# Kernel optimization log

Measured on AMD Instinct MI355X. Metric: run time of the kernel, lower is better.

Reference implementation:

```python
import jax, jax.numpy as jnp
import numpy as np

B, N, E, D = 32, 512, 2048, 128
N_STEPS = 3


def setup_inputs() -> dict:
    key = jax.random.key(0)
    ks = jax.random.split(key, 16)
    s = 0.05
    return {
        "prop_state": jax.random.normal(ks[0], (B, N, D), jnp.float32),
        "edge_states": jax.random.normal(ks[1], (B, E, D), jnp.float32),
        "A": jax.random.uniform(ks[2], (B, N, E), jnp.float32) / E,
        "tem_features": jax.random.normal(ks[3], (B, 64), jnp.float32),
        "link_W": jax.random.normal(ks[4], (D, D), jnp.float32) * s,
        "link_b": jnp.zeros((D,), jnp.float32),
        "reset_W": jax.random.normal(ks[5], (2 * D, D), jnp.float32) * s,
        "reset_b": jnp.zeros((D,), jnp.float32),
        "update_W": jax.random.normal(ks[6], (2 * D, D), jnp.float32) * s,
        "update_b": jnp.zeros((D,), jnp.float32),
        "trans_W": jax.random.normal(ks[7], (2 * D, D), jnp.float32) * s,
        "trans_b": jnp.zeros((D,), jnp.float32),
        "att_W1": jax.random.normal(ks[8], (D, D), jnp.float32) * s,
        "att_b1": jnp.zeros((D,), jnp.float32),
        "att_W2": jax.random.normal(ks[9], (D, 1), jnp.float32) * s,
        "att_b2": jnp.zeros((1,), jnp.float32),
        "out_W": jax.random.normal(ks[10], (D, D), jnp.float32) * s,
        "out_b": jnp.zeros((D,), jnp.float32),
    }


def reference(prop_state, edge_states, A, tem_features,
              link_W, link_b, reset_W, reset_b, update_W, update_b,
              trans_W, trans_b, att_W1, att_b1, att_W2, att_b2, out_W, out_b):
    init_node = prop_state
    init_edge = edge_states
    for _ in range(N_STEPS):
        edge_states = edge_states @ link_W + link_b              # [B,E,D]
        a_cur = jnp.einsum('bne,bed->bnd', A, edge_states)       # [B,N,D]
        a = jnp.concatenate([a_cur, prop_state], axis=2)         # [B,N,2D]
        r = jax.nn.sigmoid(a @ reset_W + reset_b)
        z = jax.nn.sigmoid(a @ update_W + update_b)
        joined = jnp.concatenate([a_cur, r * prop_state], axis=2)
        h_hat = jnp.tanh(joined @ trans_W + trans_b)
        prop_state = (1.0 - z) * prop_state + z * h_hat
    # attention pooling
    atten = jnp.tanh(prop_state @ att_W1 + att_b1) @ att_W2 + att_b2   # [B,N,1]
    Aw = jax.nn.softmax(jnp.transpose(atten, (0, 2, 1)), axis=2)       # [B,1,N]
    out = jnp.tanh(prop_state @ out_W + out_b)                         # [B,N,D]
    mul = jnp.einsum('bqn,bnd->bqd', Aw, out)                          # [B,1,D]
    graph_out = jnp.tanh(jnp.squeeze(mul, axis=1))                     # [B,D]
    # residual block: mean over concatenated node+edge initial states
    feat = jnp.concatenate([init_node, init_edge], axis=1)             # [B,N+E,D]
    residual = jnp.mean(feat, axis=1)                                  # [B,D]
    res = jax.nn.relu(graph_out + residual)
    return res, mul, edge_states
```

## Files before the change

kernel.cpp:

```cpp
#include <hip/hip_runtime.h>
#include <hip/hip_bf16.h>


typedef unsigned short u16;
typedef __attribute__((ext_vector_type(4))) float f32x4;
typedef __attribute__((ext_vector_type(8))) short bf16x8;

#define DI static __device__ __forceinline__

DI u16 f2bf(float f) {
    unsigned u = __builtin_bit_cast(unsigned, f);
    return (u16)((u + 0x7fffu + ((u >> 16) & 1u)) >> 16);
}

DI bf16x8 cvt8(float4 a, float4 b) {
    u16 tmp[8] = {f2bf(a.x), f2bf(a.y), f2bf(a.z), f2bf(a.w),
                  f2bf(b.x), f2bf(b.y), f2bf(b.z), f2bf(b.w)};
    return *(const bf16x8*)tmp;
}

DI int imgIdx(int k, int n) {
    return (((k >> 5) * 128 + n) * 4 + (((k >> 3) & 3) ^ ((n >> 1) & 3))) * 8 + (k & 7);
}
DI bf16x8 wfragG(const u16* __restrict__ img, int kc, int tt, int l15, int quad) {
    return *(const bf16x8*)&img[(((kc * 128 + tt * 16 + l15) * 4) + (quad ^ ((l15 >> 1) & 3))) * 8];
}

#define MFMA16(a, b, c) __builtin_amdgcn_mfma_f32_16x16x32_bf16(a, b, c, 0, 0, 0)

__global__ __launch_bounds__(256) void k_prep1(
    const float* __restrict__ linkW, const float* __restrict__ resetW,
    const float* __restrict__ updateW, const float* __restrict__ transW,
    const float* __restrict__ attW1, const float* __restrict__ outW,
    float* __restrict__ W2, u16* __restrict__ linkImg, u16* __restrict__ WrImg,
    u16* __restrict__ WzImg, u16* __restrict__ WhImg, u16* __restrict__ attW1Img,
    u16* __restrict__ outWImg)
{
    int blk = blockIdx.x, t = threadIdx.x;
    if (blk < 256) {
        int idx = blk * 256 + t;
        int out = idx >> 2, q = idx & 3;
        int r = out >> 7, c = out & 127;
        const float* ar = linkW + r * 128 + q * 32;
        float acc = 0.f;
#pragma unroll
        for (int k = 0; k < 32; k++) acc += ar[k] * linkW[(q * 32 + k) * 128 + c];
        acc += __shfl_xor(acc, 1);
        acc += __shfl_xor(acc, 2);
        if (q == 0) W2[out] = acc;
    } else {
        const float* src; u16* dst; int base;
        if (blk < 260)      { src = resetW;  dst = WrImg;    base = 256; }
        else if (blk < 264) { src = updateW; dst = WzImg;    base = 260; }
        else if (blk < 268) { src = transW;  dst = WhImg;    base = 264; }
        else if (blk < 270) { src = linkW;   dst = linkImg;  base = 268; }
        else if (blk < 272) { src = attW1;   dst = attW1Img; base = 270; }
        else                { src = outW;    dst = outWImg;  base = 272; }
        int off = (blk - base) * 8192;
        for (int i = 0; i < 32; i++) {
            int e = off + t + i * 256;
            int k = e >> 7, n = e & 127;
            dst[imgIdx(k, n)] = f2bf(src[e]);
        }
    }
}

__global__ __launch_bounds__(256) void k_prep2(
    const float* __restrict__ linkW, const float* __restrict__ linkb,
    const float* __restrict__ W2, u16* __restrict__ W3Img, float* __restrict__ ebias)
{
    int blk = blockIdx.x, t = threadIdx.x;
    if (blk < 256) {
        int idx = blk * 256 + t;
        int out = idx >> 2, q = idx & 3;
        int r = out >> 7, c = out & 127;
        const float* ar = W2 + r * 128 + q * 32;
        float acc = 0.f;
#pragma unroll
        for (int k = 0; k < 32; k++) acc += ar[k] * linkW[(q * 32 + k) * 128 + c];
        acc += __shfl_xor(acc, 1);
        acc += __shfl_xor(acc, 2);
        if (q == 0) W3Img[imgIdx(r, c)] = f2bf(acc);
    } else if (t < 128) {
        float acc = linkb[t];
#pragma unroll 8
        for (int k = 0; k < 128; k++) acc += linkb[k] * (W2[k * 128 + t] + linkW[k * 128 + t]);
        ebias[t] = acc;
    }
}

__global__ __launch_bounds__(256) void k_te(
    const float* __restrict__ E0, u16* __restrict__ Eswz, float* __restrict__ resid)
{
    __shared__ alignas(16) u16 sT[4096];
    __shared__ float sCol[128];
    int t = threadIdx.x, kc = blockIdx.x, b = blockIdx.y;
    const float* Eb = E0 + (size_t)b * 262144 + (size_t)kc * 32 * 128;
    if (t < 128) sCol[t] = 0.f;
    float part[4] = {0.f, 0.f, 0.f, 0.f};
    int ncol = (t & 31) * 4;
    for (int i = 0; i < 4; i++) {
        int f4i = t + i * 256;
        int k5 = f4i >> 5;
        float4 v = *(const float4*)&Eb[k5 * 128 + ncol];
        int g = k5 >> 3, o = k5 & 7;
        float vv[4] = {v.x, v.y, v.z, v.w};
#pragma unroll
        for (int j = 0; j < 4; j++) {
            int n = ncol + j;
            sT[(n * 4 + (g ^ ((n >> 1) & 3))) * 8 + o] = f2bf(vv[j]);
            part[j] += vv[j];
        }
    }
    __syncthreads();
#pragma unroll
    for (int j = 0; j < 4; j++) atomicAdd(&sCol[ncol + j], part[j]);
    u16* dst = Eswz + (size_t)b * 262144 + (size_t)kc * 4096;
    ((uint4*)dst)[t] = ((const uint4*)sT)[t];
    ((uint4*)dst)[t + 256] = ((const uint4*)sT)[t + 256];
    __syncthreads();
    if (t < 128) atomicAdd(&resid[b * 128 + t], sCol[t]);
}

__global__ __launch_bounds__(256, 2) void k_main(
    const float* __restrict__ A, const u16* __restrict__ Eswz,
    const float* __restrict__ p0,
    const u16* __restrict__ linkImg, const u16* __restrict__ WrImg,
    const u16* __restrict__ WzImg, const u16* __restrict__ WhImg,
    const u16* __restrict__ attW1Img, const u16* __restrict__ outWImg,
    const float* __restrict__ link_b, const float* __restrict__ reset_b,
    const float* __restrict__ update_b, const float* __restrict__ trans_b,
    const float* __restrict__ att_b1, const float* __restrict__ att_W2,
    const float* __restrict__ att_b2, const float* __restrict__ out_b,
    float* __restrict__ atten, float* __restrict__ outPool,
    float* __restrict__ resid)
{
    __shared__ float sAcc[4][16][128];
    __shared__ float sRs[4][16];
    __shared__ alignas(16) u16 sBuf[48 * 136];
    __shared__ float sRed[16];

    int t = threadIdx.x, wid = t >> 6, lane = t & 63, l15 = lane & 15, quad = lane >> 4;
    int bx = blockIdx.x;
    int g = bx >> 8, rmod = bx & 255;
    int b = (rmod & 7) + 8 * g;
    int s = (rmod >> 3) & 31;
    size_t r0 = (size_t)b * 512 + (size_t)s * 16;

    {
        const u16* Eb = Eswz + (size_t)b * 262144;
        const float* Ar = A + (r0 + l15) * 2048;
        int kbase = wid * 16;

        f32x4 acc[8];
#pragma unroll
        for (int i = 0; i < 8; i++) acc[i] = (f32x4){0.f, 0.f, 0.f, 0.f};
        float rsum = 0.f;

        float4 xc = *(const float4*)&Ar[kbase * 32 + quad * 8];
        float4 yc = *(const float4*)&Ar[kbase * 32 + quad * 8 + 4];
        bf16x8 bc[8];
#pragma unroll
        for (int tt = 0; tt < 8; tt++) bc[tt] = wfragG(Eb, kbase, tt, l15, quad);

        for (int kc = 0; kc < 16; kc++) {
            int kg = kbase + kc;
            float4 xn, yn; bf16x8 bn[8];
            if (kc < 15) {
                xn = *(const float4*)&Ar[(kg + 1) * 32 + quad * 8];
                yn = *(const float4*)&Ar[(kg + 1) * 32 + quad * 8 + 4];
#pragma unroll
                for (int tt = 0; tt < 8; tt++) bn[tt] = wfragG(Eb, kg + 1, tt, l15, quad);
            }
            rsum += xc.x + xc.y + xc.z + xc.w + yc.x + yc.y + yc.z + yc.w;
            bf16x8 af = cvt8(xc, yc);
#pragma unroll
            for (int tt = 0; tt < 8; tt++) acc[tt] = MFMA16(af, bc[tt], acc[tt]);
            if (kc < 15) {
                xc = xn; yc = yn;
#pragma unroll
                for (int tt = 0; tt < 8; tt++) bc[tt] = bn[tt];
            }
        }
        rsum += __shfl_xor(rsum, 16);
        rsum += __shfl_xor(rsum, 32);
        if (quad == 0) sRs[wid][l15] = rsum;
#pragma unroll
        for (int tt = 0; tt < 8; tt++)
#pragma unroll
            for (int r = 0; r < 4; r++)
                sAcc[wid][quad * 4 + r][tt * 16 + l15] = acc[tt][r];
    }
    __syncthreads();
    {
        int row = t >> 4, c8 = (t & 15) * 8;
        u16 o[8];
#pragma unroll
        for (int j = 0; j < 8; j++) {
            float v = sAcc[0][row][c8 + j] + sAcc[1][row][c8 + j] +
                      sAcc[2][row][c8 + j] + sAcc[3][row][c8 + j];
            o[j] = f2bf(v);
        }
        *(uint4*)&sBuf[row * 136 + c8] = *(const uint4*)o;
        float4 x = *(const float4*)&p0[(r0 + row) * 128 + c8];
        float4 y = *(const float4*)&p0[(r0 + row) * 128 + c8 + 4];
        bf16x8 pv = cvt8(x, y);
        *(bf16x8*)&sBuf[(16 + row) * 136 + c8] = pv;
    }
    if (t < 16) sRed[t] = sRs[0][t] + sRs[1][t] + sRs[2][t] + sRs[3][t];
    __syncthreads();

    int ttA = wid * 2, ttB = wid * 2 + 1;
    int colA = ttA * 16 + l15, colB = ttB * 16 + l15;

    f32x4 pS[2];
#pragma unroll
    for (int j = 0; j < 2; j++)
#pragma unroll
        for (int r = 0; r < 4; r++)
            pS[j][r] = p0[(r0 + quad * 4 + r) * 128 + (wid * 2 + j) * 16 + l15];
    {
        float s0 = pS[0][0] + pS[0][1] + pS[0][2] + pS[0][3];
        float s1 = pS[1][0] + pS[1][1] + pS[1][2] + pS[1][3];
        s0 += __shfl_xor(s0, 16); s0 += __shfl_xor(s0, 32);
        s1 += __shfl_xor(s1, 16); s1 += __shfl_xor(s1, 32);
        if (quad == 0) {
            atomicAdd(&resid[b * 128 + colA], s0);
            atomicAdd(&resid[b * 128 + colB], s1);
        }
    }
    float sv[4];
#pragma unroll
    for (int r = 0; r < 4; r++) sv[r] = sRed[quad * 4 + r];
    float lbA = link_b[colA], lbB = link_b[colB];
    float rbA = reset_b[colA], rbB = reset_b[colB];
    float ubA = update_b[colA], ubB = update_b[colB];
    float tbA = trans_b[colA], tbB = trans_b[colB];

    __syncthreads();
    if (t < 16) sRed[t] = 0.f;

    f32x4 zero4 = {0.f, 0.f, 0.f, 0.f};
    int fcol = quad * 8;
    for (int step = 0; step < 3; step++) {
        f32x4 cA = zero4, cB = zero4;
#pragma unroll 2
        for (int kc = 0; kc < 4; kc++) {
            bf16x8 af = *(const bf16x8*)&sBuf[l15 * 136 + kc * 32 + fcol];
            cA = MFMA16(af, wfragG(linkImg, kc, ttA, l15, quad), cA);
            cB = MFMA16(af, wfragG(linkImg, kc, ttB, l15, quad), cB);
        }
        __syncthreads();
#pragma unroll
        for (int r = 0; r < 4; r++) {
            sBuf[(quad * 4 + r) * 136 + colA] = f2bf(cA[r] + sv[r] * lbA);
            sBuf[(quad * 4 + r) * 136 + colB] = f2bf(cB[r] + sv[r] * lbB);
        }
        __syncthreads();
        f32x4 rA = zero4, rB = zero4, zA = zero4, zB = zero4;
#pragma unroll 2
        for (int kc = 0; kc < 8; kc++) {
            int row = ((kc >> 2) * 16 + l15) * 136 + (kc & 3) * 32 + fcol;
            bf16x8 af = *(const bf16x8*)&sBuf[row];
            rA = MFMA16(af, wfragG(WrImg, kc, ttA, l15, quad), rA);
            rB = MFMA16(af, wfragG(WrImg, kc, ttB, l15, quad), rB);
            zA = MFMA16(af, wfragG(WzImg, kc, ttA, l15, quad), zA);
            zB = MFMA16(af, wfragG(WzImg, kc, ttB, l15, quad), zB);
        }
#pragma unroll
        for (int r = 0; r < 4; r++) {
            float rvA = 1.f / (1.f + __expf(-(rA[r] + rbA)));
            float rvB = 1.f / (1.f + __expf(-(rB[r] + rbB)));
            zA[r] = 1.f / (1.f + __expf(-(zA[r] + ubA)));
            zB[r] = 1.f / (1.f + __expf(-(zB[r] + ubB)));
            sBuf[(32 + quad * 4 + r) * 136 + colA] = f2bf(rvA * pS[0][r]);
            sBuf[(32 + quad * 4 + r) * 136 + colB] = f2bf(rvB * pS[1][r]);
        }
        __syncthreads();
        f32x4 hA = zero4, hB = zero4;
#pragma unroll 2
        for (int kc = 0; kc < 8; kc++) {
            int row = ((kc >> 2) * 32 + l15) * 136 + (kc & 3) * 32 + fcol;
            bf16x8 af = *(const bf16x8*)&sBuf[row];
            hA = MFMA16(af, wfragG(WhImg, kc, ttA, l15, quad), hA);
            hB = MFMA16(af, wfragG(WhImg, kc, ttB, l15, quad), hB);
        }
#pragma unroll
        for (int r = 0; r < 4; r++) {
            float h1 = tanhf(hA[r] + tbA), h2 = tanhf(hB[r] + tbB);
            pS[0][r] = (1.f - zA[r]) * pS[0][r] + zA[r] * h1;
            pS[1][r] = (1.f - zB[r]) * pS[1][r] + zB[r] * h2;
            sBuf[(16 + quad * 4 + r) * 136 + colA] = f2bf(pS[0][r]);
            sBuf[(16 + quad * 4 + r) * 136 + colB] = f2bf(pS[1][r]);
        }
        __syncthreads();
    }
    f32x4 atA = zero4, atB = zero4, oA = zero4, oB = zero4;
#pragma unroll 2
    for (int kc = 0; kc < 4; kc++) {
        bf16x8 pf = *(const bf16x8*)&sBuf[(16 + l15) * 136 + kc * 32 + fcol];
        atA = MFMA16(pf, wfragG(attW1Img, kc, ttA, l15, quad), atA);
        atB = MFMA16(pf, wfragG(attW1Img, kc, ttB, l15, quad), atB);
        oA  = MFMA16(pf, wfragG(outWImg,  kc, ttA, l15, quad), oA);
        oB  = MFMA16(pf, wfragG(outWImg,  kc, ttB, l15, quad), oB);
    }
    float b1A = att_b1[colA], b1B = att_b1[colB];
    float w2A = att_W2[colA], w2B = att_W2[colB];
    float obA = out_b[colA],  obB = out_b[colB];
    float pr[4];
#pragma unroll
    for (int r = 0; r < 4; r++) {
        pr[r] = tanhf(atA[r] + b1A) * w2A + tanhf(atB[r] + b1B) * w2B;
        outPool[(r0 + quad * 4 + r) * 128 + colA] = tanhf(oA[r] + obA);
        outPool[(r0 + quad * 4 + r) * 128 + colB] = tanhf(oB[r] + obB);
    }
#pragma unroll
    for (int r = 0; r < 4; r++) {
        float v = pr[r];
        v += __shfl_xor(v, 1); v += __shfl_xor(v, 2);
        v += __shfl_xor(v, 4); v += __shfl_xor(v, 8);
        if (l15 == 0) atomicAdd(&sRed[quad * 4 + r], v);
    }
    __syncthreads();
    if (t < 16) atten[r0 + t] = sRed[t] + att_b2[0];
}

__global__ __launch_bounds__(64) void k_eout(
    const float* __restrict__ E0, const u16* __restrict__ W3Img,
    const float* __restrict__ ebias, float* __restrict__ Eout)
{
    int t = threadIdx.x, l15 = t & 15, quad = t >> 4;
    size_t r0 = (size_t)blockIdx.x * 16;
    bf16x8 eF[4];
#pragma unroll
    for (int kc = 0; kc < 4; kc++) {
        float4 x = *(const float4*)&E0[(r0 + l15) * 128 + kc * 32 + quad * 8];
        float4 y = *(const float4*)&E0[(r0 + l15) * 128 + kc * 32 + quad * 8 + 4];
        eF[kc] = cvt8(x, y);
    }
    f32x4 acc[8];
#pragma unroll
    for (int i = 0; i < 8; i++) acc[i] = (f32x4){0.f, 0.f, 0.f, 0.f};
    {
        bf16x8 wc[8], wn[8];
#pragma unroll
        for (int tt = 0; tt < 8; tt++) wc[tt] = wfragG(W3Img, 0, tt, l15, quad);
#pragma unroll
        for (int kc = 0; kc < 4; kc++) {
            if (kc < 3)
#pragma unroll
                for (int tt = 0; tt < 8; tt++) wn[tt] = wfragG(W3Img, kc + 1, tt, l15, quad);
#pragma unroll
            for (int tt = 0; tt < 8; tt++) acc[tt] = MFMA16(eF[kc], wc[tt], acc[tt]);
            if (kc < 3)
#pragma unroll
                for (int tt = 0; tt < 8; tt++) wc[tt] = wn[tt];
        }
    }
#pragma unroll
    for (int tt = 0; tt < 8; tt++) {
        int col = tt * 16 + l15; float eb = ebias[col];
#pragma unroll
        for (int r = 0; r < 4; r++)
            Eout[(r0 + quad * 4 + r) * 128 + col] = acc[tt][r] + eb;
    }
}

__global__ __launch_bounds__(512) void k_fin(
    const float* __restrict__ atten, const float* __restrict__ outPool,
    const float* __restrict__ resid,
    float* __restrict__ outRes, float* __restrict__ outMul)
{
    __shared__ float swv[512];
    __shared__ float sred[512];
    __shared__ float sacc[4][128];
    int t = threadIdx.x, b = blockIdx.x;
    float a = atten[b * 512 + t];
    sred[t] = a; __syncthreads();
    for (int s = 256; s > 0; s >>= 1) { if (t < s) sred[t] = fmaxf(sred[t], sred[t + s]); __syncthreads(); }
    float mx = sred[0]; __syncthreads();
    float e = __expf(a - mx);
    swv[t] = e; sred[t] = e; __syncthreads();
    for (int s = 256; s > 0; s >>= 1) { if (t < s) sred[t] += sred[t + s]; __syncthreads(); }
    float Z = sred[0]; __syncthreads();
    int col = t & 127, q = t >> 7;
    const float* op = outPool + ((size_t)b * 512 + q * 128) * 128 + col;
    float accM = 0.f;
#pragma unroll 8
    for (int n = 0; n < 128; n++) accM += swv[q * 128 + n] * op[(size_t)n * 128];
    sacc[q][col] = accM;
    __syncthreads();
    if (t < 128) {
        float mulv = (sacc[0][t] + sacc[1][t] + sacc[2][t] + sacc[3][t]) / Z;
        float rv = resid[b * 128 + t] * (1.f / 2560.f);
        outMul[b * 128 + t] = mulv;
        outRes[b * 128 + t] = fmaxf(0.f, tanhf(mulv) + rv);
    }
}

extern "C" void kernel_launch(void* const* d_in, const int* in_sizes, int n_in,
                              void* d_out, int out_size, void* d_ws, size_t ws_size,
                              hipStream_t stream)
{
    const float* prop0  = (const float*)d_in[0];
    const float* edge0  = (const float*)d_in[1];
    const float* Amat   = (const float*)d_in[2];
    const float* linkW  = (const float*)d_in[4];
    const float* linkb  = (const float*)d_in[5];
    const float* resetW = (const float*)d_in[6];
    const float* resetb = (const float*)d_in[7];
    const float* updateW= (const float*)d_in[8];
    const float* updateb= (const float*)d_in[9];
    const float* transW = (const float*)d_in[10];
    const float* transb = (const float*)d_in[11];
    const float* attW1  = (const float*)d_in[12];
    const float* attb1  = (const float*)d_in[13];
    const float* attW2  = (const float*)d_in[14];
    const float* attb2  = (const float*)d_in[15];
    const float* outW   = (const float*)d_in[16];
    const float* outb   = (const float*)d_in[17];

    char* w = (char*)d_ws;
    float* ws_atten   = (float*)(w + 4259840);
    float* ws_resid   = (float*)(w + 4325376);
    float* ws_W2      = (float*)(w + 4341760);
    float* ws_ebias   = (float*)(w + 4407296);
    u16*   ws_linkImg = (u16*)(w + 4407808);
    u16*   ws_W3Img   = (u16*)(w + 4440576);
    u16*   ws_WrImg   = (u16*)(w + 4473344);
    u16*   ws_WzImg   = (u16*)(w + 4538880);
    u16*   ws_WhImg   = (u16*)(w + 4604416);
    u16*   ws_attW1Img= (u16*)(w + 4669952);
    u16*   ws_outWImg = (u16*)(w + 4702720);

    float* out_res  = (float*)d_out;
    float* out_mul  = out_res + 4096;
    float* out_edge = out_res + 8192;
    u16*   Eswz     = (u16*)out_edge;
    float* outPool  = out_edge + 4194304;

    hipMemsetAsync(ws_resid, 0, 32 * 128 * sizeof(float), stream);
    k_prep1<<<274, 256, 0, stream>>>(linkW, resetW, updateW, transW, attW1, outW,
                                     ws_W2, ws_linkImg, ws_WrImg, ws_WzImg, ws_WhImg,
                                     ws_attW1Img, ws_outWImg);
    k_prep2<<<257, 256, 0, stream>>>(linkW, linkb, ws_W2, ws_W3Img, ws_ebias);
    k_te<<<dim3(64, 32), 256, 0, stream>>>(edge0, Eswz, ws_resid);
    k_main<<<1024, 256, 0, stream>>>(Amat, Eswz, prop0,
                                     ws_linkImg, ws_WrImg, ws_WzImg, ws_WhImg,
                                     ws_attW1Img, ws_outWImg,
                                     linkb, resetb, updateb, transb,
                                     attb1, attW2, attb2, outb,
                                     ws_atten, outPool, ws_resid);
    k_fin<<<32, 512, 0, stream>>>(ws_atten, outPool, ws_resid, out_res, out_mul);
    k_eout<<<4096, 64, 0, stream>>>(edge0, ws_W3Img, ws_ebias, out_edge);
}
```

Before: 376.6 us.

## Split A@E across column and K halves to shrink shared memory and raise occupancy

Reworks the A·E reduction so each wave owns 4 output column tiles over half of K, instead of all 8 tiles over a quarter of K. The cross-wave reduction shrinks from a 4-way 32KB shared buffer to a 2-way padded buffer, and the kernel now requests 4 blocks per CU instead of 2. Each wave runs twice as many K iterations, so A loads are duplicated across the column groups. One barrier is dropped, but the lower register budget may cause spills.

```diff
diff --git a/kernel.cpp b/kernel.cpp
--- a/kernel.cpp
+++ b/kernel.cpp
@@ -122,7 +122,7 @@
     if (t < 128) atomicAdd(&resid[b * 128 + t], sCol[t]);
 }
 
-__global__ __launch_bounds__(256, 2) void k_main(
+__global__ __launch_bounds__(256, 4) void k_main(
     const float* __restrict__ A, const u16* __restrict__ Eswz,
     const float* __restrict__ p0,
     const u16* __restrict__ linkImg, const u16* __restrict__ WrImg,
@@ -135,12 +135,13 @@
     float* __restrict__ atten, float* __restrict__ outPool,
     float* __restrict__ resid)
 {
-    __shared__ float sAcc[4][16][128];
-    __shared__ float sRs[4][16];
+    __shared__ float sAcc2[2][16 * 65];
+    __shared__ float sRs[2][16];
     __shared__ alignas(16) u16 sBuf[48 * 136];
     __shared__ float sRed[16];
 
     int t = threadIdx.x, wid = t >> 6, lane = t & 63, l15 = lane & 15, quad = lane >> 4;
+    int tg = wid >> 1, kh = wid & 1;
     int bx = blockIdx.x;
     int g = bx >> 8, rmod = bx & 255;
     int b = (rmod & 7) + 8 * g;
@@ -149,65 +150,70 @@
 
     {
         const u16* Eb = Eswz + (size_t)b * 262144;
-        const float* Ar = A + (r0 + l15) * 2048;
-        int kbase = wid * 16;
-
-        f32x4 acc[8];
-#pragma unroll
-        for (int i = 0; i < 8; i++) acc[i] = (f32x4){0.f, 0.f, 0.f, 0.f};
+        const float* Ar = A + (r0 + l15) * 2048 + kh * 1024;
+
+        f32x4 acc[4];
+#pragma unroll
+        for (int i = 0; i < 4; i++) acc[i] = (f32x4){0.f, 0.f, 0.f, 0.f};
         float rsum = 0.f;
 
-        float4 xc = *(const float4*)&Ar[kbase * 32 + quad * 8];
-        float4 yc = *(const float4*)&Ar[kbase * 32 + quad * 8 + 4];
-        bf16x8 bc[8];
-#pragma unroll
-        for (int tt = 0; tt < 8; tt++) bc[tt] = wfragG(Eb, kbase, tt, l15, quad);
-
-        for (int kc = 0; kc < 16; kc++) {
-            int kg = kbase + kc;
-            float4 xn, yn; bf16x8 bn[8];
-            if (kc < 15) {
-                xn = *(const float4*)&Ar[(kg + 1) * 32 + quad * 8];
-                yn = *(const float4*)&Ar[(kg + 1) * 32 + quad * 8 + 4];
-#pragma unroll
-                for (int tt = 0; tt < 8; tt++) bn[tt] = wfragG(Eb, kg + 1, tt, l15, quad);
+        float4 xc = *(const float4*)&Ar[quad * 8];
+        float4 yc = *(const float4*)&Ar[quad * 8 + 4];
+        bf16x8 bc[4];
+#pragma unroll
+        for (int tt = 0; tt < 4; tt++) bc[tt] = wfragG(Eb, kh * 32, tg * 4 + tt, l15, quad);
+
+        for (int kc = 0; kc < 32; kc++) {
+            int kg = kh * 32 + kc;
+            float4 xn, yn; bf16x8 bn[4];
+            if (kc < 31) {
+                xn = *(const float4*)&Ar[(kc + 1) * 32 + quad * 8];
+                yn = *(const float4*)&Ar[(kc + 1) * 32 + quad * 8 + 4];
+#pragma unroll
+                for (int tt = 0; tt < 4; tt++) bn[tt] = wfragG(Eb, kg + 1, tg * 4 + tt, l15, quad);
             }
             rsum += xc.x + xc.y + xc.z + xc.w + yc.x + yc.y + yc.z + yc.w;
             bf16x8 af = cvt8(xc, yc);
 #pragma unroll
-            for (int tt = 0; tt < 8; tt++) acc[tt] = MFMA16(af, bc[tt], acc[tt]);
-            if (kc < 15) {
+            for (int tt = 0; tt < 4; tt++) acc[tt] = MFMA16(af, bc[tt], acc[tt]);
+            if (kc < 31) {
                 xc = xn; yc = yn;
 #pragma unroll
-                for (int tt = 0; tt < 8; tt++) bc[tt] = bn[tt];
+                for (int tt = 0; tt < 4; tt++) bc[tt] = bn[tt];
             }
         }
         rsum += __shfl_xor(rsum, 16);
         rsum += __shfl_xor(rsum, 32);
-        if (quad == 0) sRs[wid][l15] = rsum;
-#pragma unroll
-        for (int tt = 0; tt < 8; tt++)
-#pragma unroll
-            for (int r = 0; r < 4; r++)
-                sAcc[wid][quad * 4 + r][tt * 16 + l15] = acc[tt][r];
-    }
-    __syncthreads();
-    {
-        int row = t >> 4, c8 = (t & 15) * 8;
-        u16 o[8];
-#pragma unroll
-        for (int j = 0; j < 8; j++) {
-            float v = sAcc[0][row][c8 + j] + sAcc[1][row][c8 + j] +
-                      sAcc[2][row][c8 + j] + sAcc[3][row][c8 + j];
-            o[j] = f2bf(v);
-        }
-        *(uint4*)&sBuf[row * 136 + c8] = *(const uint4*)o;
-        float4 x = *(const float4*)&p0[(r0 + row) * 128 + c8];
-        float4 y = *(const float4*)&p0[(r0 + row) * 128 + c8 + 4];
-        bf16x8 pv = cvt8(x, y);
-        *(bf16x8*)&sBuf[(16 + row) * 136 + c8] = pv;
-    }
-    if (t < 16) sRed[t] = sRs[0][t] + sRs[1][t] + sRs[2][t] + sRs[3][t];
+        if (quad == 0 && tg == 0) sRs[kh][l15] = rsum;
+        if (kh == 1) {
+#pragma unroll
+            for (int tt = 0; tt < 4; tt++)
+#pragma unroll
+                for (int r = 0; r < 4; r++)
+                    sAcc2[tg][(quad * 4 + r) * 65 + tt * 16 + l15] = acc[tt][r];
+        }
+        if (t < 16) sRed[t] = 0.f;
+        __syncthreads();
+        if (kh == 0) {
+#pragma unroll
+            for (int tt = 0; tt < 4; tt++)
+#pragma unroll
+                for (int r = 0; r < 4; r++) {
+                    float v = acc[tt][r] + sAcc2[tg][(quad * 4 + r) * 65 + tt * 16 + l15];
+                    sBuf[(quad * 4 + r) * 136 + tg * 64 + tt * 16 + l15] = f2bf(v);
+                }
+        } else {
+            int idx = tg * 64 + lane;
+            int row = idx >> 3, c8 = (idx & 7) * 16;
+            const float* pr = &p0[(r0 + row) * 128 + c8];
+            float4 x0 = *(const float4*)&pr[0];
+            float4 y0 = *(const float4*)&pr[4];
+            float4 x1 = *(const float4*)&pr[8];
+            float4 y1 = *(const float4*)&pr[12];
+            *(bf16x8*)&sBuf[(16 + row) * 136 + c8] = cvt8(x0, y0);
+            *(bf16x8*)&sBuf[(16 + row) * 136 + c8 + 8] = cvt8(x1, y1);
+        }
+    }
     __syncthreads();
 
     int ttA = wid * 2, ttB = wid * 2 + 1;
@@ -231,14 +237,11 @@
     }
     float sv[4];
 #pragma unroll
-    for (int r = 0; r < 4; r++) sv[r] = sRed[quad * 4 + r];
+    for (int r = 0; r < 4; r++) sv[r] = sRs[0][quad * 4 + r] + sRs[1][quad * 4 + r];
     float lbA = link_b[colA], lbB = link_b[colB];
     float rbA = reset_b[colA], rbB = reset_b[colB];
     float ubA = update_b[colA], ubB = update_b[colB];
     float tbA = trans_b[colA], tbB = trans_b[colB];
-
-    __syncthreads();
-    if (t < 16) sRed[t] = 0.f;
 
     f32x4 zero4 = {0.f, 0.f, 0.f, 0.f};
     int fcol = quad * 8;
```

Result: no change. 369.4 us (-1.9%).
